# Kernel optimization log

Measured on AMD Instinct MI355X. Metric: run time of the kernel, lower is better.

The kernel has to match this reference:

```python
import jax, jax.numpy as jnp
import numpy as np

HIDDEN = 512
HEADS = 8
PREFIX = 1  # prefix_size: rows >= PREFIX may not attend to cols < PREFIX (except causal tril already zeroed those only partially)


def setup_inputs() -> dict:
    key = jax.random.key(0)
    k1, k2, k3 = jax.random.split(key, 3)
    B, L, D = 2, 4096, HIDDEN
    x = jax.random.normal(k1, (B, L, D), dtype=jnp.float32)
    # torch Linear(hidden, 3*hidden): y = x @ W^T + b; we store W^T directly as [D, 3D]
    w_in = jax.random.normal(k2, (D, 3 * D), dtype=jnp.float32) * (1.0 / np.sqrt(D))
    b_in = jnp.zeros((3 * D,), dtype=jnp.float32)
    w_out = jax.random.normal(k3, (D, D), dtype=jnp.float32) * (1.0 / np.sqrt(D))
    b_out = jnp.zeros((D,), dtype=jnp.float32)
    return {"x": x, "w_in": w_in, "b_in": b_in, "w_out": w_out, "b_out": b_out}


def _prefix_causal_mask(L):
    # tril(ones) then zero out [prefix:, :prefix]
    m = jnp.tril(jnp.ones((L, L), dtype=bool))
    m = m.at[PREFIX:, :PREFIX].set(False)
    return m  # True = attend allowed


def reference(x, w_in, b_in, w_out, b_out):
    B, L, D = x.shape
    H, hd = HEADS, D // HEADS
    qkv = x @ w_in + b_in  # [B, L, 3D]
    q, k, v = jnp.split(qkv, 3, axis=-1)
    q = q.reshape(B, L, H, hd).transpose(0, 2, 1, 3)  # [B,H,L,hd]
    k = k.reshape(B, L, H, hd).transpose(0, 2, 1, 3)
    v = v.reshape(B, L, H, hd).transpose(0, 2, 1, 3)
    scale = 1.0 / np.sqrt(hd).astype(np.float32)
    attn = jnp.einsum('bhqd,bhkd->bhqk', q, k) * scale  # [B,H,L,L]
    mask = _prefix_causal_mask(L)
    attn = jnp.where(mask[None, None, :, :], attn, -jnp.inf)
    attn = jax.nn.softmax(attn, axis=-1)  # dropout p=0.0 -> identity
    out = jnp.einsum('bhqk,bhkd->bhqd', attn, v)  # [B,H,L,hd]
    out = out.transpose(0, 2, 1, 3).reshape(B, L, D)
    return out @ w_out + b_out
```

## Files before the change

### kernel.cpp

```cpp
#include <hip/hip_runtime.h>
#include <hip/hip_bf16.h>

#define BSZ   2
#define LSEQ  4096
#define DH    512
#define NH    8
#define HDIM  64

typedef unsigned short ushort_t;
typedef __attribute__((ext_vector_type(8))) short s8v;
typedef __attribute__((ext_vector_type(4))) short s4v;
typedef __attribute__((ext_vector_type(4))) float f4v;

#define C_EXP 0.18033688011112042f

__device__ __forceinline__ ushort_t f2bf(float f) {
    __hip_bfloat16 h = __float2bfloat16(f);
    return *(ushort_t*)&h;
}

__device__ __forceinline__ unsigned int fbits(float f) {
    union { float f; unsigned int u; } c; c.f = f; return c.u;
}

__device__ __forceinline__ unsigned int pk_trunc(float lo, float hi) {
    return (fbits(lo) >> 16) | (fbits(hi) & 0xFFFF0000u);
}

__device__ __forceinline__ void gld_lds16(const ushort_t* g, ushort_t* l) {
    __builtin_amdgcn_global_load_lds(
        (const __attribute__((address_space(1))) void*)g,
        (__attribute__((address_space(3))) void*)l, 16, 0, 0);
}

__device__ __forceinline__ void transpose_tile(const float* __restrict__ src,
                                               ushort_t* __restrict__ dst,
                                               int R, int C, int bx, int by)
{
    __shared__ float tile[32][33];
    int r0 = by * 32, c0 = bx * 32;
    int t = threadIdx.x;
    int tr = t >> 5, tc = t & 31;
    #pragma unroll
    for (int i = 0; i < 4; i++)
        tile[tr + 8 * i][tc] = src[(size_t)(r0 + tr + 8 * i) * C + c0 + tc];
    __syncthreads();
    #pragma unroll
    for (int i = 0; i < 4; i++) {
        int oc = tr + 8 * i;
        dst[(size_t)(c0 + oc) * R + r0 + tc] = f2bf(tile[tc][oc]);
    }
}

__global__ __launch_bounds__(256) void prep(const float* __restrict__ x,
                                            ushort_t* __restrict__ xb,
                                            const float* __restrict__ w_in,
                                            ushort_t* __restrict__ w_inT,
                                            const float* __restrict__ w_out,
                                            ushort_t* __restrict__ w_outT,
                                            float* __restrict__ Oacc,
                                            float* __restrict__ lacc)
{
    int bx = blockIdx.x;
    if (bx < 4096) {
        int i = (bx * 256 + threadIdx.x) * 4;
        float4 v = *(const float4*)&x[i];
        ushort_t o[4] = {f2bf(v.x), f2bf(v.y), f2bf(v.z), f2bf(v.w)};
        *(uint2*)&xb[i] = *(uint2*)o;
    } else if (bx < 4864) {
        int idx = bx - 4096;
        transpose_tile(w_in, w_inT, DH, 3 * DH, idx % 48, idx / 48);
    } else if (bx < 5120) {
        int idx = bx - 4864;
        transpose_tile(w_out, w_outT, DH, DH, idx % 16, idx / 16);
    } else if (bx < 9216) {
        int i = ((bx - 5120) * 256 + threadIdx.x) * 4;
        float4 z = {0.f, 0.f, 0.f, 0.f};
        *(float4*)&Oacc[i] = z;
    } else {
        int i = ((bx - 9216) * 256 + threadIdx.x) * 4;
        float4 z = {0.f, 0.f, 0.f, 0.f};
        *(float4*)&lacc[i] = z;
    }
}

template <typename OUT, bool QSCALE, bool VTRANS>
__global__ __launch_bounds__(256) void gemm_bt(const ushort_t* __restrict__ A,
                                               const ushort_t* __restrict__ Bt,
                                               const float* __restrict__ bias,
                                               OUT* __restrict__ C,
                                               ushort_t* __restrict__ vtout,
                                               int M, int N, int K)
{
    __shared__ ushort_t As[128 * 32];
    __shared__ ushort_t Bs[128 * 32];
    const int tid = threadIdx.x;
    const int row0 = blockIdx.y * 128, col0 = blockIdx.x * 128;
    const int wid = tid >> 6, lane = tid & 63;
    const int wm = wid >> 1, wn = wid & 1;
    const int quad = lane >> 4, ln = lane & 15;

    f4v acc[4][4] = {};

    const int srow = (lane >> 2);
    const int scol = (lane & 3) * 8;

    for (int k0 = 0; k0 < K; k0 += 32) {
        #pragma unroll
        for (int t = 0; t < 2; t++) {
            int chunk = wid * 2 + t;
            int r = chunk * 16 + srow;
            gld_lds16(&A[(size_t)(row0 + r) * K + k0 + scol], &As[chunk * 512]);
            gld_lds16(&Bt[(size_t)(col0 + r) * K + k0 + scol], &Bs[chunk * 512]);
        }
        __syncthreads();
        s8v af[4], bf[4];
        #pragma unroll
        for (int mt = 0; mt < 4; mt++)
            af[mt] = *(const s8v*)&As[(wm * 64 + mt * 16 + ln) * 32 + quad * 8];
        #pragma unroll
        for (int nt = 0; nt < 4; nt++)
            bf[nt] = *(const s8v*)&Bs[(wn * 64 + nt * 16 + ln) * 32 + quad * 8];
        #pragma unroll
        for (int mt = 0; mt < 4; mt++)
            #pragma unroll
            for (int nt = 0; nt < 4; nt++)
                acc[mt][nt] = __builtin_amdgcn_mfma_f32_16x16x32_bf16(
                    af[mt], bf[nt], acc[mt][nt], 0, 0, 0);
        __syncthreads();
    }

    #pragma unroll
    for (int mt = 0; mt < 4; mt++) {
        #pragma unroll
        for (int nt = 0; nt < 4; nt++) {
            int c = col0 + wn * 64 + nt * 16 + ln;
            float bv = bias[c];
            float scl = 1.0f;
            if constexpr (QSCALE) scl = (c < DH) ? C_EXP : 1.0f;
            bool vcol = false;
            if constexpr (VTRANS) vcol = (c >= 2 * DH);
            if (vcol) {
                int d = c - 2 * DH;
                int hh = d >> 6, dd = d & 63;
                int r0 = row0 + wm * 64 + mt * 16 + quad * 4;
                int bb = r0 >> 12, l = r0 & (LSEQ - 1);
                ushort_t tmp[4];
                #pragma unroll
                for (int reg = 0; reg < 4; reg++)
                    tmp[reg] = f2bf(acc[mt][nt][reg] + bv);
                *(uint2*)&vtout[((size_t)((bb * NH + hh) * 64 + dd)) * LSEQ + l]
                    = *(uint2*)tmp;
            } else {
                #pragma unroll
                for (int reg = 0; reg < 4; reg++) {
                    int r = row0 + wm * 64 + mt * 16 + quad * 4 + reg;
                    float v = (acc[mt][nt][reg] + bv) * scl;
                    if constexpr (sizeof(OUT) == 2)
                        C[(size_t)r * N + c] = (OUT)f2bf(v);
                    else
                        C[(size_t)r * N + c] = v;
                }
            }
        }
    }
}

__global__ __launch_bounds__(128) void flash_mfma(const ushort_t* __restrict__ qkv,
                                                  const ushort_t* __restrict__ vt,
                                                  float* __restrict__ Oacc,
                                                  float* __restrict__ lacc)
{
    __shared__ ushort_t Ks[64 * 72];
    __shared__ ushort_t Vs[64 * 72];

    const int p  = blockIdx.x >> 2;
    const int kq = blockIdx.x & 3;
    const int h = blockIdx.y, b = blockIdx.z;
    const int tid = threadIdx.x;
    const int w = tid >> 6, lane = tid & 63;
    const int quad = lane >> 4, ln = lane & 15;

    const int sr = tid >> 1, sc = (tid & 1) * 32;
    const int ldsw = sr * 72 + sc;
    const size_t kstep = (size_t)64 * 3 * DH;

    const int qts[2] = {63 - p, p};

    for (int ti = 0; ti < 2; ti++) {
        const int qt = qts[ti], q0 = qt * 64;
        const int qrow0 = q0 + w * 32;
        const int n = qt + 1;
        const int ktBeg = (n * kq) >> 2;
        const int ktEnd = (n * (kq + 1)) >> 2;

        s8v qa[2][2];
        #pragma unroll
        for (int qg = 0; qg < 2; qg++) {
            const ushort_t* qrow = qkv
                + ((size_t)(b * LSEQ + qrow0 + qg * 16 + ln)) * (3 * DH) + h * HDIM;
            qa[qg][0] = *(const s8v*)(qrow + quad * 8);
            qa[qg][1] = *(const s8v*)(qrow + 32 + quad * 8);
        }

        float l_s[2] = {0.0f, 0.0f};
        f4v o_acc[2][4] = {};

        if (ktBeg < ktEnd) {
            size_t gk = ((size_t)(b * LSEQ + ktBeg * 64 + sr)) * (3 * DH) + DH + h * HDIM + sc;
            size_t gv = ((size_t)((b * NH + h) * 64 + sr)) * LSEQ + ktBeg * 64 + sc;
            uint4 pk0 = *(const uint4*)&qkv[gk];
            uint4 pk1 = *(const uint4*)&qkv[gk + 8];
            uint4 pk2 = *(const uint4*)&qkv[gk + 16];
            uint4 pk3 = *(const uint4*)&qkv[gk + 24];
            uint4 pv0 = *(const uint4*)&vt[gv];
            uint4 pv1 = *(const uint4*)&vt[gv + 8];
            uint4 pv2 = *(const uint4*)&vt[gv + 16];
            uint4 pv3 = *(const uint4*)&vt[gv + 24];

            for (int kt = ktBeg; kt < ktEnd; kt++) {
                const int k0 = kt * 64;
                __syncthreads();
                *(uint4*)&Ks[ldsw]      = pk0;
                *(uint4*)&Ks[ldsw + 8]  = pk1;
                *(uint4*)&Ks[ldsw + 16] = pk2;
                *(uint4*)&Ks[ldsw + 24] = pk3;
                *(uint4*)&Vs[ldsw]      = pv0;
                *(uint4*)&Vs[ldsw + 8]  = pv1;
                *(uint4*)&Vs[ldsw + 16] = pv2;
                *(uint4*)&Vs[ldsw + 24] = pv3;
                if (kt + 1 < ktEnd) {
                    gk += kstep; gv += 64;
                    pk0 = *(const uint4*)&qkv[gk];
                    pk1 = *(const uint4*)&qkv[gk + 8];
                    pk2 = *(const uint4*)&qkv[gk + 16];
                    pk3 = *(const uint4*)&qkv[gk + 24];
                    pv0 = *(const uint4*)&vt[gv];
                    pv1 = *(const uint4*)&vt[gv + 8];
                    pv2 = *(const uint4*)&vt[gv + 16];
                    pv3 = *(const uint4*)&vt[gv + 24];
                }
                __syncthreads();

                s8v kb[4][2];
                #pragma unroll
                for (int nt = 0; nt < 4; nt++) {
                    kb[nt][0] = *(const s8v*)&Ks[(nt * 16 + ln) * 72 + quad * 8];
                    kb[nt][1] = *(const s8v*)&Ks[(nt * 16 + ln) * 72 + 32 + quad * 8];
                }
                s4v vf[4][4];
                #pragma unroll
                for (int dt = 0; dt < 4; dt++)
                    #pragma unroll
                    for (int nt = 0; nt < 4; nt++)
                        vf[dt][nt] = *(const s4v*)&Vs[(dt * 16 + ln) * 72 + nt * 16 + quad * 4];

                #pragma unroll
                for (int qg = 0; qg < 2; qg++) {
                    f4v s[4] = {};
                    #pragma unroll
                    for (int nt = 0; nt < 4; nt++) {
                        s[nt] = __builtin_amdgcn_mfma_f32_16x16x32_bf16(kb[nt][0], qa[qg][0], s[nt], 0, 0, 0);
                        s[nt] = __builtin_amdgcn_mfma_f32_16x16x32_bf16(kb[nt][1], qa[qg][1], s[nt], 0, 0, 0);
                    }

                    float pp[4][4];
                    const int q = qrow0 + qg * 16 + ln;
                    if (kt == qt) {
                        #pragma unroll
                        for (int nt = 0; nt < 4; nt++) {
                            #pragma unroll
                            for (int reg = 0; reg < 4; reg++) {
                                int kidx = k0 + nt * 16 + quad * 4 + reg;
                                bool valid = (kidx <= q) && (kidx >= 1 || q == 0);
                                pp[nt][reg] = valid ? __builtin_amdgcn_exp2f(s[nt][reg]) : 0.0f;
                            }
                        }
                    } else {
                        #pragma unroll
                        for (int nt = 0; nt < 4; nt++)
                            #pragma unroll
                            for (int reg = 0; reg < 4; reg++)
                                pp[nt][reg] = __builtin_amdgcn_exp2f(s[nt][reg]);
                        if (kt == 0 && quad == 0)
                            pp[0][0] = 0.0f;
                    }

                    #pragma unroll
                    for (int nt = 0; nt < 4; nt++)
                        l_s[qg] += (pp[nt][0] + pp[nt][1]) + (pp[nt][2] + pp[nt][3]);

                    #pragma unroll
                    for (int nt = 0; nt < 4; nt++) {
                        union { unsigned int u[2]; s4v v; } pk;
                        pk.u[0] = pk_trunc(pp[nt][0], pp[nt][1]);
                        pk.u[1] = pk_trunc(pp[nt][2], pp[nt][3]);
                        #pragma unroll
                        for (int dt = 0; dt < 4; dt++)
                            o_acc[qg][dt] = __builtin_amdgcn_mfma_f32_16x16x16bf16_1k(
                                pk.v, vf[dt][nt], o_acc[qg][dt], 0, 0, 0);
                    }
                }
            }
        }

        #pragma unroll
        for (int qg = 0; qg < 2; qg++) {
            float lf = l_s[qg];
            lf += __shfl_xor(lf, 16);
            lf += __shfl_xor(lf, 32);
            if (quad == 0)
                atomicAdd(&lacc[((size_t)(b * NH + h)) * LSEQ + qrow0 + qg * 16 + ln], lf);
            #pragma unroll
            for (int dt = 0; dt < 4; dt++)
                #pragma unroll
                for (int reg = 0; reg < 4; reg++)
                    atomicAdd(&Oacc[((size_t)(b * LSEQ + qrow0 + qg * 16 + quad * 4 + reg)) * DH
                                    + h * HDIM + dt * 16 + ln],
                              o_acc[qg][dt][reg]);
        }
    }
}

__global__ __launch_bounds__(256) void normalize(const float* __restrict__ Oacc,
                                                 const float* __restrict__ lacc,
                                                 ushort_t* __restrict__ att)
{
    int t = blockIdx.x * 256 + threadIdx.x;
    int row = t >> 5;
    int col0 = (t & 31) * 16;
    int h = col0 >> 6;
    int b = row >> 12, l = row & (LSEQ - 1);
    float linv = 1.0f / lacc[((size_t)(b * NH + h)) * LSEQ + l];
    const float* o = &Oacc[(size_t)row * DH + col0];
    ushort_t tmp[16];
    #pragma unroll
    for (int j = 0; j < 16; j++) tmp[j] = f2bf(o[j] * linv);
    size_t g = (size_t)row * DH + col0;
    *(uint4*)&att[g]     = *(uint4*)&tmp[0];
    *(uint4*)&att[g + 8] = *(uint4*)&tmp[8];
}

extern "C" void kernel_launch(void* const* d_in, const int* in_sizes, int n_in,
                              void* d_out, int out_size, void* d_ws, size_t ws_size,
                              hipStream_t stream)
{
    const float* x     = (const float*)d_in[0];
    const float* w_in  = (const float*)d_in[1];
    const float* b_in  = (const float*)d_in[2];
    const float* w_out = (const float*)d_in[3];
    const float* b_out = (const float*)d_in[4];
    float* out = (float*)d_out;

    const int M = BSZ * LSEQ;
    char* ws = (char*)d_ws;
    ushort_t* xb    = (ushort_t*)ws;                       ws += (size_t)M * DH * 2;
    ushort_t* w_inT = (ushort_t*)ws;                       ws += (size_t)3 * DH * DH * 2;
    ushort_t* w_outT= (ushort_t*)ws;                       ws += (size_t)DH * DH * 2;
    ushort_t* qkvb  = (ushort_t*)ws;                       ws += (size_t)M * 3 * DH * 2;
    ushort_t* vtb   = (ushort_t*)ws;                       ws += (size_t)M * DH * 2;
    ushort_t* attb  = (ushort_t*)ws;                       ws += (size_t)M * DH * 2;
    float*    Oacc  = (float*)ws;                          ws += (size_t)M * DH * 4;
    float*    lacc  = (float*)ws;

    prep<<<9280, 256, 0, stream>>>(x, xb, w_in, w_inT, w_out, w_outT, Oacc, lacc);

    gemm_bt<ushort_t, true, true><<<dim3(3 * DH / 128, M / 128), 256, 0, stream>>>(
        xb, w_inT, b_in, qkvb, vtb, M, 3 * DH, DH);

    flash_mfma<<<dim3(128, NH, BSZ), 128, 0, stream>>>(qkvb, vtb, Oacc, lacc);

    normalize<<<1024, 256, 0, stream>>>(Oacc, lacc, attb);

    gemm_bt<float, false, false><<<dim3(DH / 128, M / 128), 256, 0, stream>>>(
        attb, w_outT, b_out, out, nullptr, M, DH, DH);
}
```

Before: 202.8 us.

## Fuse split-K flash reduction and normalize into attention kernel via LDS

Replaces the 4-way split-KV attention with global atomic accumulation by a 2-way in-block split. Four waves run per block: two pairs each take half the KV tiles and combine their partial O and l through shared memory. The kernel then normalizes and writes bf16 output directly, removing the Oacc/lacc zeroing in prep, the float atomics, and the separate normalize kernel. The trade is fewer blocks (512 instead of 2048), so occupancy and load balance drop. Waves on the shorter half also idle at barriers when the tile count is odd.

Result: slower. 219.2 us (+8.1%).

```diff
diff --git a/kernel.cpp b/kernel.cpp
--- a/kernel.cpp
+++ b/kernel.cpp
@@ -57,9 +57,7 @@
                                             const float* __restrict__ w_in,
                                             ushort_t* __restrict__ w_inT,
                                             const float* __restrict__ w_out,
-                                            ushort_t* __restrict__ w_outT,
-                                            float* __restrict__ Oacc,
-                                            float* __restrict__ lacc)
+                                            ushort_t* __restrict__ w_outT)
 {
     int bx = blockIdx.x;
     if (bx < 4096) {
@@ -70,17 +68,9 @@
     } else if (bx < 4864) {
         int idx = bx - 4096;
         transpose_tile(w_in, w_inT, DH, 3 * DH, idx % 48, idx / 48);
-    } else if (bx < 5120) {
+    } else {
         int idx = bx - 4864;
         transpose_tile(w_out, w_outT, DH, DH, idx % 16, idx / 16);
-    } else if (bx < 9216) {
-        int i = ((bx - 5120) * 256 + threadIdx.x) * 4;
-        float4 z = {0.f, 0.f, 0.f, 0.f};
-        *(float4*)&Oacc[i] = z;
-    } else {
-        int i = ((bx - 9216) * 256 + threadIdx.x) * 4;
-        float4 z = {0.f, 0.f, 0.f, 0.f};
-        *(float4*)&lacc[i] = z;
     }
 }
 
@@ -166,22 +156,24 @@
     }
 }
 
-__global__ __launch_bounds__(128) void flash_mfma(const ushort_t* __restrict__ qkv,
+__global__ __launch_bounds__(256) void flash_mfma(const ushort_t* __restrict__ qkv,
                                                   const ushort_t* __restrict__ vt,
-                                                  float* __restrict__ Oacc,
-                                                  float* __restrict__ lacc)
-{
-    __shared__ ushort_t Ks[64 * 72];
-    __shared__ ushort_t Vs[64 * 72];
-
-    const int p  = blockIdx.x >> 2;
-    const int kq = blockIdx.x & 3;
+                                                  ushort_t* __restrict__ att)
+{
+    __shared__ ushort_t Ks[2][64 * 72];
+    __shared__ ushort_t Vs[2][64 * 72];
+    __shared__ f4v   Osc[2][8][64];
+    __shared__ float Lsc[2][2][64];
+
+    const int p = blockIdx.x;
     const int h = blockIdx.y, b = blockIdx.z;
     const int tid = threadIdx.x;
     const int w = tid >> 6, lane = tid & 63;
+    const int khalf = w >> 1, wrow = w & 1;
     const int quad = lane >> 4, ln = lane & 15;
 
-    const int sr = tid >> 1, sc = (tid & 1) * 32;
+    const int ptid = tid & 127;
+    const int sr = ptid >> 1, sc = (ptid & 1) * 32;
     const int ldsw = sr * 72 + sc;
     const size_t kstep = (size_t)64 * 3 * DH;
 
@@ -189,10 +181,11 @@
 
     for (int ti = 0; ti < 2; ti++) {
         const int qt = qts[ti], q0 = qt * 64;
-        const int qrow0 = q0 + w * 32;
+        const int qrow0 = q0 + wrow * 32;
         const int n = qt + 1;
-        const int ktBeg = (n * kq) >> 2;
-        const int ktEnd = (n * (kq + 1)) >> 2;
+        const int half = (n + 1) >> 1;
+        const int ktBeg = khalf ? half : 0;
+        const int ktEnd = khalf ? n : half;
 
         s8v qa[2][2];
         #pragma unroll
@@ -206,54 +199,62 @@
         float l_s[2] = {0.0f, 0.0f};
         f4v o_acc[2][4] = {};
 
-        if (ktBeg < ktEnd) {
-            size_t gk = ((size_t)(b * LSEQ + ktBeg * 64 + sr)) * (3 * DH) + DH + h * HDIM + sc;
-            size_t gv = ((size_t)((b * NH + h) * 64 + sr)) * LSEQ + ktBeg * 64 + sc;
-            uint4 pk0 = *(const uint4*)&qkv[gk];
-            uint4 pk1 = *(const uint4*)&qkv[gk + 8];
-            uint4 pk2 = *(const uint4*)&qkv[gk + 16];
-            uint4 pk3 = *(const uint4*)&qkv[gk + 24];
-            uint4 pv0 = *(const uint4*)&vt[gv];
-            uint4 pv1 = *(const uint4*)&vt[gv + 8];
-            uint4 pv2 = *(const uint4*)&vt[gv + 16];
-            uint4 pv3 = *(const uint4*)&vt[gv + 24];
-
-            for (int kt = ktBeg; kt < ktEnd; kt++) {
-                const int k0 = kt * 64;
-                __syncthreads();
-                *(uint4*)&Ks[ldsw]      = pk0;
-                *(uint4*)&Ks[ldsw + 8]  = pk1;
-                *(uint4*)&Ks[ldsw + 16] = pk2;
-                *(uint4*)&Ks[ldsw + 24] = pk3;
-                *(uint4*)&Vs[ldsw]      = pv0;
-                *(uint4*)&Vs[ldsw + 8]  = pv1;
-                *(uint4*)&Vs[ldsw + 16] = pv2;
-                *(uint4*)&Vs[ldsw + 24] = pv3;
-                if (kt + 1 < ktEnd) {
-                    gk += kstep; gv += 64;
-                    pk0 = *(const uint4*)&qkv[gk];
-                    pk1 = *(const uint4*)&qkv[gk + 8];
-                    pk2 = *(const uint4*)&qkv[gk + 16];
-                    pk3 = *(const uint4*)&qkv[gk + 24];
-                    pv0 = *(const uint4*)&vt[gv];
-                    pv1 = *(const uint4*)&vt[gv + 8];
-                    pv2 = *(const uint4*)&vt[gv + 16];
-                    pv3 = *(const uint4*)&vt[gv + 24];
-                }
-                __syncthreads();
-
+        size_t gk = ((size_t)(b * LSEQ + ktBeg * 64 + sr)) * (3 * DH) + DH + h * HDIM + sc;
+        size_t gv = ((size_t)((b * NH + h) * 64 + sr)) * LSEQ + ktBeg * 64 + sc;
+        uint4 pk0 = *(const uint4*)&qkv[gk];
+        uint4 pk1 = *(const uint4*)&qkv[gk + 8];
+        uint4 pk2 = *(const uint4*)&qkv[gk + 16];
+        uint4 pk3 = *(const uint4*)&qkv[gk + 24];
+        uint4 pv0 = *(const uint4*)&vt[gv];
+        uint4 pv1 = *(const uint4*)&vt[gv + 8];
+        uint4 pv2 = *(const uint4*)&vt[gv + 16];
+        uint4 pv3 = *(const uint4*)&vt[gv + 24];
+
+        int kt = ktBeg;
+        for (int it = 0; it < half; it++, kt++) {
+            const bool active = (kt < ktEnd);
+            const int k0 = kt * 64;
+            __syncthreads();
+            if (active) {
+                ushort_t* Kb = &Ks[khalf][0];
+                ushort_t* Vb = &Vs[khalf][0];
+                *(uint4*)&Kb[ldsw]      = pk0;
+                *(uint4*)&Kb[ldsw + 8]  = pk1;
+                *(uint4*)&Kb[ldsw + 16] = pk2;
+                *(uint4*)&Kb[ldsw + 24] = pk3;
+                *(uint4*)&Vb[ldsw]      = pv0;
+                *(uint4*)&Vb[ldsw + 8]  = pv1;
+                *(uint4*)&Vb[ldsw + 16] = pv2;
+                *(uint4*)&Vb[ldsw + 24] = pv3;
+            }
+            if (kt + 1 < ktEnd) {
+                gk += kstep; gv += 64;
+                pk0 = *(const uint4*)&qkv[gk];
+                pk1 = *(const uint4*)&qkv[gk + 8];
+                pk2 = *(const uint4*)&qkv[gk + 16];
+                pk3 = *(const uint4*)&qkv[gk + 24];
+                pv0 = *(const uint4*)&vt[gv];
+                pv1 = *(const uint4*)&vt[gv + 8];
+                pv2 = *(const uint4*)&vt[gv + 16];
+                pv3 = *(const uint4*)&vt[gv + 24];
+            }
+            __syncthreads();
+
+            if (active) {
+                const ushort_t* Kb = &Ks[khalf][0];
+                const ushort_t* Vb = &Vs[khalf][0];
                 s8v kb[4][2];
                 #pragma unroll
                 for (int nt = 0; nt < 4; nt++) {
-                    kb[nt][0] = *(const s8v*)&Ks[(nt * 16 + ln) * 72 + quad * 8];
-                    kb[nt][1] = *(const s8v*)&Ks[(nt * 16 + ln) * 72 + 32 + quad * 8];
+                    kb[nt][0] = *(const s8v*)&Kb[(nt * 16 + ln) * 72 + quad * 8];
+                    kb[nt][1] = *(const s8v*)&Kb[(nt * 16 + ln) * 72 + 32 + quad * 8];
                 }
                 s4v vf[4][4];
                 #pragma unroll
                 for (int dt = 0; dt < 4; dt++)
                     #pragma unroll
                     for (int nt = 0; nt < 4; nt++)
-                        vf[dt][nt] = *(const s4v*)&Vs[(dt * 16 + ln) * 72 + nt * 16 + quad * 4];
+                        vf[dt][nt] = *(const s4v*)&Vb[(dt * 16 + ln) * 72 + nt * 16 + quad * 4];
 
                 #pragma unroll
                 for (int qg = 0; qg < 2; qg++) {
@@ -304,41 +305,38 @@
             }
         }
 
-        #pragma unroll
-        for (int qg = 0; qg < 2; qg++) {
-            float lf = l_s[qg];
-            lf += __shfl_xor(lf, 16);
-            lf += __shfl_xor(lf, 32);
-            if (quad == 0)
-                atomicAdd(&lacc[((size_t)(b * NH + h)) * LSEQ + qrow0 + qg * 16 + ln], lf);
+        if (w >= 2) {
             #pragma unroll
-            for (int dt = 0; dt < 4; dt++)
-                #pragma unroll
-                for (int reg = 0; reg < 4; reg++)
-                    atomicAdd(&Oacc[((size_t)(b * LSEQ + qrow0 + qg * 16 + quad * 4 + reg)) * DH
-                                    + h * HDIM + dt * 16 + ln],
-                              o_acc[qg][dt][reg]);
-        }
-    }
-}
-
-__global__ __launch_bounds__(256) void normalize(const float* __restrict__ Oacc,
-                                                 const float* __restrict__ lacc,
-                                                 ushort_t* __restrict__ att)
-{
-    int t = blockIdx.x * 256 + threadIdx.x;
-    int row = t >> 5;
-    int col0 = (t & 31) * 16;
-    int h = col0 >> 6;
-    int b = row >> 12, l = row & (LSEQ - 1);
-    float linv = 1.0f / lacc[((size_t)(b * NH + h)) * LSEQ + l];
-    const float* o = &Oacc[(size_t)row * DH + col0];
-    ushort_t tmp[16];
-    #pragma unroll
-    for (int j = 0; j < 16; j++) tmp[j] = f2bf(o[j] * linv);
-    size_t g = (size_t)row * DH + col0;
-    *(uint4*)&att[g]     = *(uint4*)&tmp[0];
-    *(uint4*)&att[g + 8] = *(uint4*)&tmp[8];
+            for (int qg = 0; qg < 2; qg++) {
+                #pragma unroll
+                for (int dt = 0; dt < 4; dt++)
+                    Osc[wrow][qg * 4 + dt][lane] = o_acc[qg][dt];
+                Lsc[wrow][qg][lane] = l_s[qg];
+            }
+        }
+        __syncthreads();
+        if (w < 2) {
+            #pragma unroll
+            for (int qg = 0; qg < 2; qg++) {
+                float lf = l_s[qg] + Lsc[w][qg][lane];
+                lf += __shfl_xor(lf, 16);
+                lf += __shfl_xor(lf, 32);
+                #pragma unroll
+                for (int dt = 0; dt < 4; dt++)
+                    o_acc[qg][dt] += Osc[w][qg * 4 + dt][lane];
+                #pragma unroll
+                for (int reg = 0; reg < 4; reg++) {
+                    float lr = __shfl(lf, quad * 4 + reg);
+                    float linv = 1.0f / lr;
+                    size_t row = (size_t)(b * LSEQ + qrow0 + qg * 16 + quad * 4 + reg);
+                    #pragma unroll
+                    for (int dt = 0; dt < 4; dt++)
+                        att[row * DH + h * HDIM + dt * 16 + ln]
+                            = f2bf(o_acc[qg][dt][reg] * linv);
+                }
+            }
+        }
+    }
 }
 
 extern "C" void kernel_launch(void* const* d_in, const int* in_sizes, int n_in,
@@ -359,18 +357,14 @@
     ushort_t* w_outT= (ushort_t*)ws;                       ws += (size_t)DH * DH * 2;
     ushort_t* qkvb  = (ushort_t*)ws;                       ws += (size_t)M * 3 * DH * 2;
     ushort_t* vtb   = (ushort_t*)ws;                       ws += (size_t)M * DH * 2;
-    ushort_t* attb  = (ushort_t*)ws;                       ws += (size_t)M * DH * 2;
-    float*    Oacc  = (float*)ws;                          ws += (size_t)M * DH * 4;
-    float*    lacc  = (float*)ws;
-
-    prep<<<9280, 256, 0, stream>>>(x, xb, w_in, w_inT, w_out, w_outT, Oacc, lacc);
+    ushort_t* attb  = (ushort_t*)ws;
+
+    prep<<<5120, 256, 0, stream>>>(x, xb, w_in, w_inT, w_out, w_outT);
 
     gemm_bt<ushort_t, true, true><<<dim3(3 * DH / 128, M / 128), 256, 0, stream>>>(
         xb, w_inT, b_in, qkvb, vtb, M, 3 * DH, DH);
 
-    flash_mfma<<<dim3(128, NH, BSZ), 128, 0, stream>>>(qkvb, vtb, Oacc, lacc);
-
-    normalize<<<1024, 256, 0, stream>>>(Oacc, lacc, attb);
+    flash_mfma<<<dim3(32, NH, BSZ), 256, 0, stream>>>(qkvb, vtb, attb);
 
     gemm_bt<float, false, false><<<dim3(DH / 128, M / 128), 256, 0, stream>>>(
         attb, w_outT, b_out, out, nullptr, M, DH, DH);
```
